# Optimization experiments

Measured on AMD Instinct MI355X. Metric: run time of the kernel, lower is better.

Reference implementation:

```python
import jax, jax.numpy as jnp
import numpy as np

VOCAB = 1_000_000
EMBED_DIM = 128
BATCH = 16_384
NOISE_COUNT = 16


def setup_inputs() -> dict:
    key = jax.random.key(0)
    k1, k2, k3, k4, k5, k6 = jax.random.split(key, 6)
    embed = jax.random.uniform(k1, (EMBED_DIM, VOCAB), jnp.float32, -1.0, 1.0)
    bias = jax.random.uniform(k2, (VOCAB, 1), jnp.float32, -1.0, 1.0)
    u = jax.random.uniform(k3, (VOCAB,), jnp.float32, 1e-3, 1.0)
    freq = u / u.sum()  # normalized unigram^0.75 noise distribution
    targets = jax.random.randint(k4, (BATCH,), 0, VOCAB)
    contexts = jax.random.randint(k5, (BATCH,), 0, VOCAB)
    noises = jax.random.randint(k6, (BATCH * NOISE_COUNT,), 0, VOCAB)
    return {"embed": embed, "bias": bias, "freq": freq,
            "targets": targets, "contexts": contexts, "noises": noises,
            "noise_count": NOISE_COUNT}


def reference(embed, bias, freq, targets, contexts, noises, noise_count):
    # embed: (E, V); bias: (V, 1); freq: (V,)
    E = embed.shape[0]
    B = targets.shape[0]
    re = 10.0
    q = embed[:, targets]                      # (E, B) target embeddings
    r = embed[:, contexts]                     # (E, B) context embeddings
    b = bias[targets, 0][None, :]              # (1, B)
    s = ((r * q).sum(0)[None, :] + b) / E      # (1, B) scaled score
    # positive term: log(sigmoid(s - log(k * p(target))))
    pos = jax.nn.log_sigmoid(s - jnp.log(noise_count * freq[targets]))
    loss = pos.sum()
    # noise term: log(1 - sigmoid(tile(s,k) - log(k * p(noise)))) = log_sigmoid(-x)
    s_tiled = jnp.tile(s, (1, noise_count))    # (1, B*k) == torch.cat((s,)*k, dim=1)
    noise_loss = jax.nn.log_sigmoid(-(s_tiled - jnp.log(noise_count * freq[noises]))).sum()
    total_loss = -(loss + noise_loss) / B
    penalty = re * ((q * q).sum() + (r * r).sum()) / (E * B)
    return total_loss + penalty
```

## Files before the change

### kernel.cpp

```cpp
#include <hip/hip_runtime.h>
#include <hip/hip_bf16.h>
#include <math.h>


#define NB 2048

struct alignas(16) bf16x8 { __hip_bfloat16 h[8]; };

__device__ __forceinline__ float log_sigmoid_f(float x) {
    return fminf(x, 0.0f) - log1pf(expf(-fabsf(x)));
}

__device__ __forceinline__ int task_col(int i, const int* __restrict__ targets,
                                        const int* __restrict__ contexts) {
    const int pair = i >> 1;
    return (i & 1) ? contexts[pair] : targets[pair];
}

__global__ __launch_bounds__(256) void hist_kernel(
    const int* __restrict__ targets, const int* __restrict__ contexts,
    int* __restrict__ counts, int T2, int sh)
{
    const int i = blockIdx.x * 256 + threadIdx.x;
    if (i < T2) atomicAdd(&counts[task_col(i, targets, contexts) >> sh], 1);
}

__global__ __launch_bounds__(256) void scan_kernel(
    const int* __restrict__ counts, int* __restrict__ cursors, int nb)
{
    __shared__ int wv_tot[4];
    const int tid  = threadIdx.x;
    const int lane = tid & 63;
    const int w    = tid >> 6;
    int v[8];
    const int base = tid * 8;
    int local = 0;
    #pragma unroll
    for (int k = 0; k < 8; ++k) {
        const int idx = base + k;
        v[k] = (idx < nb) ? counts[idx] : 0;
        local += v[k];
    }
    int incl = local;
    #pragma unroll
    for (int off = 1; off < 64; off <<= 1) {
        const int n = __shfl_up(incl, off, 64);
        if (lane >= off) incl += n;
    }
    if (lane == 63) wv_tot[w] = incl;
    __syncthreads();
    int wpre = 0;
    for (int i = 0; i < w; ++i) wpre += wv_tot[i];
    int run = wpre + incl - local;
    #pragma unroll
    for (int k = 0; k < 8; ++k) {
        const int idx = base + k;
        if (idx < nb) cursors[idx] = run;
        run += v[k];
    }
}

__global__ __launch_bounds__(256) void scatter_kernel(
    const int* __restrict__ targets, const int* __restrict__ contexts,
    int* __restrict__ cursors, int* __restrict__ sorted,
    int* __restrict__ invperm, int T2, int sh)
{
    const int i = blockIdx.x * 256 + threadIdx.x;
    if (i < T2) {
        const int col = task_col(i, targets, contexts);
        const int pos = atomicAdd(&cursors[col >> sh], 1);
        sorted[pos] = i;
        invperm[i]  = pos;
    }
}

__global__ __launch_bounds__(256) void gather_kernel(
    const float* __restrict__ embed,
    const int* __restrict__ targets, const int* __restrict__ contexts,
    const int* __restrict__ sorted, bf16x8* __restrict__ dense,
    int V, int T2)
{
    const int g = threadIdx.x & 15;
    const int p = threadIdx.x >> 4;
    const int pos = blockIdx.x * 16 + p;
    if (pos >= T2) return;
    const int col = task_col(sorted[pos], targets, contexts);
    const float* src = embed + col + (size_t)(g * 8) * V;
    float v[8];
    #pragma unroll
    for (int k = 0; k < 8; ++k) v[k] = src[(size_t)k * V];
    bf16x8 outv;
    #pragma unroll
    for (int k = 0; k < 8; ++k) outv.h[k] = __float2bfloat16(v[k]);
    dense[(size_t)pos * 16 + g] = outv;
}

__global__ __launch_bounds__(256) void compute_kernel(
    const bf16x8* __restrict__ dense, const int* __restrict__ invperm,
    const float* __restrict__ bias, const float* __restrict__ freq,
    const int* __restrict__ targets, const int* __restrict__ noises,
    float* __restrict__ partials, int B, int NC)
{
    __shared__ float sh_dot[16][17];
    __shared__ float sh_sq [16][17];
    __shared__ float sh_s  [16];
    __shared__ float sh_wred[4];

    const int p = threadIdx.x & 15;
    const int g = threadIdx.x >> 4;
    const int j = blockIdx.x * 16 + p;
    const bool valid = (j < B);

    float contrib = 0.0f;
    float dot = 0.0f, sq = 0.0f;
    float lg0 = 0.0f; bool has0 = false;
    float bval = 0.0f, lgt = 0.0f;

    if (valid) {
        if (g < NC) {
            const int n = noises[j + (size_t)g * B];
            lg0 = logf((float)NC * freq[n]);
            has0 = true;
        }
        if (g == 0) {
            const int t = targets[j];
            bval = bias[t];
            lgt  = logf((float)NC * freq[t]);
        }
        const bf16x8 qv = dense[(size_t)invperm[2 * j]     * 16 + g];
        const bf16x8 rv = dense[(size_t)invperm[2 * j + 1] * 16 + g];
        #pragma unroll
        for (int k = 0; k < 8; ++k) {
            const float qe = __bfloat162float(qv.h[k]);
            const float re = __bfloat162float(rv.h[k]);
            dot = fmaf(qe, re, dot);
            sq  = fmaf(qe, qe, fmaf(re, re, sq));
        }
    }
    sh_dot[p][g] = dot;
    sh_sq [p][g] = sq;
    __syncthreads();

    if (threadIdx.x < 16) {
        float d = 0.0f, s2 = 0.0f;
        #pragma unroll
        for (int gg = 0; gg < 16; ++gg) {
            d  += sh_dot[threadIdx.x][gg];
            s2 += sh_sq [threadIdx.x][gg];
        }
        float sval = 0.0f;
        if (valid) {
            sval = (d + bval) / 128.0f;
            const float pos = log_sigmoid_f(sval - lgt);
            contrib += -pos / (float)B + 10.0f * s2 / (128.0f * (float)B);
        }
        sh_s[threadIdx.x] = sval;
    }
    __syncthreads();

    if (valid) {
        const float sval = sh_s[p];
        float nacc = 0.0f;
        if (has0) nacc = log_sigmoid_f(-(sval - lg0));
        for (int k = g + 16; k < NC; k += 16) {
            const int n = noises[j + (size_t)k * B];
            nacc += log_sigmoid_f(-(sval - logf((float)NC * freq[n])));
        }
        contrib += -nacc / (float)B;
    }

    #pragma unroll
    for (int off = 32; off > 0; off >>= 1)
        contrib += __shfl_xor(contrib, off, 64);
    if ((threadIdx.x & 63) == 0) sh_wred[threadIdx.x >> 6] = contrib;
    __syncthreads();
    if (threadIdx.x == 0)
        partials[blockIdx.x] = sh_wred[0] + sh_wred[1] + sh_wred[2] + sh_wred[3];
}

__global__ __launch_bounds__(256) void reduce_partials_kernel(
    const float* __restrict__ parts, int n, float* __restrict__ out)
{
    __shared__ double sh[256];
    double a = 0.0;
    for (int i = threadIdx.x; i < n; i += 256) a += (double)parts[i];
    sh[threadIdx.x] = a;
    __syncthreads();
    for (int s = 128; s > 0; s >>= 1) {
        if (threadIdx.x < s) sh[threadIdx.x] += sh[threadIdx.x + s];
        __syncthreads();
    }
    if (threadIdx.x == 0) out[0] = (float)sh[0];
}

__global__ __launch_bounds__(256) void nce_fallback(
    const float* __restrict__ embed, const float* __restrict__ bias,
    const float* __restrict__ freq, const int* __restrict__ targets,
    const int* __restrict__ contexts, const int* __restrict__ noises,
    float* __restrict__ block_partials, int V, int E, int B, int NC)
{
    __shared__ float sh_dot[16][17];
    __shared__ float sh_sq [16][17];
    __shared__ float sh_s  [16];
    __shared__ float sh_wred[4];
    const int p = threadIdx.x & 15;
    const int g = threadIdx.x >> 4;
    const int j = blockIdx.x * 16 + p;
    const bool valid = (j < B);
    float contrib = 0.0f, dot = 0.0f, sq = 0.0f;
    float lg0 = 0.0f; bool has0 = false; float bval = 0.0f, lgt = 0.0f;
    if (valid) {
        const int t = targets[j], c = contexts[j];
        if (g < NC) { const int n = noises[j + (size_t)g * B];
                      lg0 = logf((float)NC * freq[n]); has0 = true; }
        if (g == 0) { bval = bias[t]; lgt = logf((float)NC * freq[t]); }
        const int epc = E / 16, e0 = g * epc;
        const float* ct = embed + t; const float* cc = embed + c;
        #pragma unroll 8
        for (int e = e0; e < e0 + epc; ++e) {
            float qe = ct[(size_t)e * V], re = cc[(size_t)e * V];
            dot = fmaf(qe, re, dot);
            sq  = fmaf(qe, qe, fmaf(re, re, sq));
        }
    }
    sh_dot[p][g] = dot; sh_sq[p][g] = sq;
    __syncthreads();
    if (threadIdx.x < 16) {
        float d = 0.0f, s2 = 0.0f;
        #pragma unroll
        for (int gg = 0; gg < 16; ++gg) { d += sh_dot[threadIdx.x][gg]; s2 += sh_sq[threadIdx.x][gg]; }
        float sval = 0.0f;
        if (valid) {
            sval = (d + bval) / (float)E;
            contrib += -log_sigmoid_f(sval - lgt) / (float)B + 10.0f * s2 / ((float)E * (float)B);
        }
        sh_s[threadIdx.x] = sval;
    }
    __syncthreads();
    if (valid) {
        const float sval = sh_s[p];
        float nacc = 0.0f;
        if (has0) nacc = log_sigmoid_f(-(sval - lg0));
        for (int k = g + 16; k < NC; k += 16) {
            const int n = noises[j + (size_t)k * B];
            nacc += log_sigmoid_f(-(sval - logf((float)NC * freq[n])));
        }
        contrib += -nacc / (float)B;
    }
    #pragma unroll
    for (int off = 32; off > 0; off >>= 1) contrib += __shfl_xor(contrib, off, 64);
    if ((threadIdx.x & 63) == 0) sh_wred[threadIdx.x >> 6] = contrib;
    __syncthreads();
    if (threadIdx.x == 0)
        block_partials[blockIdx.x] = sh_wred[0] + sh_wred[1] + sh_wred[2] + sh_wred[3];
}

extern "C" void kernel_launch(void* const* d_in, const int* in_sizes, int n_in,
                              void* d_out, int out_size, void* d_ws, size_t ws_size,
                              hipStream_t stream) {
    const float* embed    = (const float*)d_in[0];
    const float* bias     = (const float*)d_in[1];
    const float* freq     = (const float*)d_in[2];
    const int*   targets  = (const int*)d_in[3];
    const int*   contexts = (const int*)d_in[4];
    const int*   noises   = (const int*)d_in[5];

    const int V  = in_sizes[2];
    const int E  = in_sizes[0] / V;
    const int B  = in_sizes[3];
    const int NC = in_sizes[5] / B;
    const int T2 = 2 * B;

    char* ws = (char*)d_ws;
    float* partials = (float*)ws;
    int*   counts   = (int*)(ws + 16384);
    int*   cursors  = counts + NB;
    int*   sorted   = cursors + NB;
    int*   invperm  = sorted + T2;
    size_t dense_off = 16384 + 2 * (size_t)NB * 4 + 2 * (size_t)T2 * 4;
    dense_off = (dense_off + 255) & ~(size_t)255;
    bf16x8* dense = (bf16x8*)(ws + dense_off);
    const size_t needed = dense_off + (size_t)T2 * 128 * 2;

    const int nblocks = (B + 15) / 16;

    if (E == 128 && (B & 15) == 0 && ws_size >= needed) {
        int sh = 0;
        while ((((V - 1) >> sh) + 1) > NB) ++sh;
        const int nb = ((V - 1) >> sh) + 1;

        hipMemsetAsync(counts, 0, (size_t)NB * 4, stream);
        hist_kernel<<<(T2 + 255) / 256, 256, 0, stream>>>(targets, contexts, counts, T2, sh);
        scan_kernel<<<1, 256, 0, stream>>>(counts, cursors, nb);
        scatter_kernel<<<(T2 + 255) / 256, 256, 0, stream>>>(targets, contexts, cursors,
                                                             sorted, invperm, T2, sh);
        gather_kernel<<<(T2 + 15) / 16, 256, 0, stream>>>(embed, targets, contexts,
                                                          sorted, dense, V, T2);
        compute_kernel<<<nblocks, 256, 0, stream>>>(dense, invperm, bias, freq,
                                                    targets, noises, partials, B, NC);
    } else {
        nce_fallback<<<nblocks, 256, 0, stream>>>(embed, bias, freq, targets, contexts,
                                                  noises, partials, V, E, B, NC);
    }
    reduce_partials_kernel<<<1, 256, 0, stream>>>(partials, nblocks, (float*)d_out);
}
```

Measured before the change: 102.2 us.

## Gather embedding rows into transposed bf16 buffer with row-parallel grid

The gather stage now gives each thread one sorted column. The grid is split across embedding-dimension slices, and each slice writes its values into a transposed (E, T2) bf16 buffer, so reads of a given embedding row across consecutive sorted columns fall near each other. The scatter stage now stores the column index itself rather than the task index, which drops one indirection in the gather. The compute kernel reads the transposed buffer with strided scalar bf16 loads instead of 16-byte vector loads, so the compute side gets less coalescing in exchange for better gather locality.

```diff
diff --git a/kernel.cpp b/kernel.cpp
--- a/kernel.cpp
+++ b/kernel.cpp
@@ -4,8 +4,7 @@
 
 
 #define NB 2048
-
-struct alignas(16) bf16x8 { __hip_bfloat16 h[8]; };
+#define ELOOP 8
 
 __device__ __forceinline__ float log_sigmoid_f(float x) {
     return fminf(x, 0.0f) - log1pf(expf(-fabsf(x)));
@@ -62,44 +61,40 @@
 
 __global__ __launch_bounds__(256) void scatter_kernel(
     const int* __restrict__ targets, const int* __restrict__ contexts,
-    int* __restrict__ cursors, int* __restrict__ sorted,
+    int* __restrict__ cursors, int* __restrict__ sorted_cols,
     int* __restrict__ invperm, int T2, int sh)
 {
     const int i = blockIdx.x * 256 + threadIdx.x;
     if (i < T2) {
         const int col = task_col(i, targets, contexts);
         const int pos = atomicAdd(&cursors[col >> sh], 1);
-        sorted[pos] = i;
+        sorted_cols[pos] = col;
         invperm[i]  = pos;
     }
 }
 
-__global__ __launch_bounds__(256) void gather_kernel(
-    const float* __restrict__ embed,
-    const int* __restrict__ targets, const int* __restrict__ contexts,
-    const int* __restrict__ sorted, bf16x8* __restrict__ dense,
-    int V, int T2)
-{
-    const int g = threadIdx.x & 15;
-    const int p = threadIdx.x >> 4;
-    const int pos = blockIdx.x * 16 + p;
+__global__ __launch_bounds__(256) void gather_rows_kernel(
+    const float* __restrict__ embed, const int* __restrict__ sorted_cols,
+    __hip_bfloat16* __restrict__ denseT, int V, int T2)
+{
+    const int pos = blockIdx.x * 256 + threadIdx.x;
     if (pos >= T2) return;
-    const int col = task_col(sorted[pos], targets, contexts);
-    const float* src = embed + col + (size_t)(g * 8) * V;
-    float v[8];
-    #pragma unroll
-    for (int k = 0; k < 8; ++k) v[k] = src[(size_t)k * V];
-    bf16x8 outv;
-    #pragma unroll
-    for (int k = 0; k < 8; ++k) outv.h[k] = __float2bfloat16(v[k]);
-    dense[(size_t)pos * 16 + g] = outv;
+    const int col = sorted_cols[pos];
+    const int e0  = blockIdx.y * ELOOP;
+    const float* src = embed + (size_t)e0 * V + col;
+    float v[ELOOP];
+    #pragma unroll
+    for (int k = 0; k < ELOOP; ++k) v[k] = src[(size_t)k * V];
+    __hip_bfloat16* dst = denseT + (size_t)e0 * T2 + pos;
+    #pragma unroll
+    for (int k = 0; k < ELOOP; ++k) dst[(size_t)k * T2] = __float2bfloat16(v[k]);
 }
 
 __global__ __launch_bounds__(256) void compute_kernel(
-    const bf16x8* __restrict__ dense, const int* __restrict__ invperm,
+    const __hip_bfloat16* __restrict__ denseT, const int* __restrict__ invperm,
     const float* __restrict__ bias, const float* __restrict__ freq,
     const int* __restrict__ targets, const int* __restrict__ noises,
-    float* __restrict__ partials, int B, int NC)
+    float* __restrict__ partials, int B, int NC, int T2)
 {
     __shared__ float sh_dot[16][17];
     __shared__ float sh_sq [16][17];
@@ -127,12 +122,14 @@
             bval = bias[t];
             lgt  = logf((float)NC * freq[t]);
         }
-        const bf16x8 qv = dense[(size_t)invperm[2 * j]     * 16 + g];
-        const bf16x8 rv = dense[(size_t)invperm[2 * j + 1] * 16 + g];
+        const int pq = invperm[2 * j];
+        const int pr = invperm[2 * j + 1];
+        const __hip_bfloat16* bq = denseT + (size_t)(g * 8) * T2 + pq;
+        const __hip_bfloat16* br = denseT + (size_t)(g * 8) * T2 + pr;
         #pragma unroll
         for (int k = 0; k < 8; ++k) {
-            const float qe = __bfloat162float(qv.h[k]);
-            const float re = __bfloat162float(rv.h[k]);
+            const float qe = __bfloat162float(bq[(size_t)k * T2]);
+            const float re = __bfloat162float(br[(size_t)k * T2]);
             dot = fmaf(qe, re, dot);
             sq  = fmaf(qe, qe, fmaf(re, re, sq));
         }
@@ -275,16 +272,16 @@
     float* partials = (float*)ws;
     int*   counts   = (int*)(ws + 16384);
     int*   cursors  = counts + NB;
-    int*   sorted   = cursors + NB;
-    int*   invperm  = sorted + T2;
+    int*   sorted_cols = cursors + NB;
+    int*   invperm  = sorted_cols + T2;
     size_t dense_off = 16384 + 2 * (size_t)NB * 4 + 2 * (size_t)T2 * 4;
     dense_off = (dense_off + 255) & ~(size_t)255;
-    bf16x8* dense = (bf16x8*)(ws + dense_off);
-    const size_t needed = dense_off + (size_t)T2 * 128 * 2;
+    __hip_bfloat16* denseT = (__hip_bfloat16*)(ws + dense_off);
+    const size_t needed = dense_off + (size_t)E * T2 * 2;
 
     const int nblocks = (B + 15) / 16;
 
-    if (E == 128 && (B & 15) == 0 && ws_size >= needed) {
+    if (E == 128 && (T2 & 255) == 0 && ws_size >= needed) {
         int sh = 0;
         while ((((V - 1) >> sh) + 1) > NB) ++sh;
         const int nb = ((V - 1) >> sh) + 1;
@@ -293,11 +290,11 @@
         hist_kernel<<<(T2 + 255) / 256, 256, 0, stream>>>(targets, contexts, counts, T2, sh);
         scan_kernel<<<1, 256, 0, stream>>>(counts, cursors, nb);
         scatter_kernel<<<(T2 + 255) / 256, 256, 0, stream>>>(targets, contexts, cursors,
-                                                             sorted, invperm, T2, sh);
-        gather_kernel<<<(T2 + 15) / 16, 256, 0, stream>>>(embed, targets, contexts,
-                                                          sorted, dense, V, T2);
-        compute_kernel<<<nblocks, 256, 0, stream>>>(dense, invperm, bias, freq,
-                                                    targets, noises, partials, B, NC);
+                                                             sorted_cols, invperm, T2, sh);
+        dim3 ggrid(T2 / 256, E / ELOOP);
+        gather_rows_kernel<<<ggrid, 256, 0, stream>>>(embed, sorted_cols, denseT, V, T2);
+        compute_kernel<<<nblocks, 256, 0, stream>>>(denseT, invperm, bias, freq,
+                                                    targets, noises, partials, B, NC, T2);
     } else {
         nce_fallback<<<nblocks, 256, 0, stream>>>(embed, bias, freq, targets, contexts,
                                                   noises, partials, V, E, B, NC);
```

New measurement: 119.3 us. 16.8% more time.

## Gather embeddings with 64 adjacent sorted columns per wave and LDS transpose

Applied to the files above, without the earlier changes.

The scatter now stores the column index directly, which removes the indirect targets/contexts lookup in the gather. The gather is restructured so that each wavefront's 64 lanes read 64 consecutive sorted columns for the same embedding row, giving nearby addresses per load instead of 16 scattered columns. Results go through a shared-memory tile and are written out as 16-byte row chunks in the existing dense layout. This adds a block barrier and an LDS round trip, and the 2D grid reloads sorted_cols once per embedding slice.

```diff
diff --git a/kernel.cpp b/kernel.cpp
--- a/kernel.cpp
+++ b/kernel.cpp
@@ -4,6 +4,8 @@
 
 
 #define NB 2048
+#define GP 64
+#define GE 32
 
 struct alignas(16) bf16x8 { __hip_bfloat16 h[8]; };
 
@@ -62,37 +64,54 @@
 
 __global__ __launch_bounds__(256) void scatter_kernel(
     const int* __restrict__ targets, const int* __restrict__ contexts,
-    int* __restrict__ cursors, int* __restrict__ sorted,
+    int* __restrict__ cursors, int* __restrict__ sorted_cols,
     int* __restrict__ invperm, int T2, int sh)
 {
     const int i = blockIdx.x * 256 + threadIdx.x;
     if (i < T2) {
         const int col = task_col(i, targets, contexts);
         const int pos = atomicAdd(&cursors[col >> sh], 1);
-        sorted[pos] = i;
+        sorted_cols[pos] = col;
         invperm[i]  = pos;
     }
 }
 
-__global__ __launch_bounds__(256) void gather_kernel(
-    const float* __restrict__ embed,
-    const int* __restrict__ targets, const int* __restrict__ contexts,
-    const int* __restrict__ sorted, bf16x8* __restrict__ dense,
-    int V, int T2)
-{
-    const int g = threadIdx.x & 15;
-    const int p = threadIdx.x >> 4;
-    const int pos = blockIdx.x * 16 + p;
-    if (pos >= T2) return;
-    const int col = task_col(sorted[pos], targets, contexts);
-    const float* src = embed + col + (size_t)(g * 8) * V;
+__global__ __launch_bounds__(256) void gather_t_kernel(
+    const float* __restrict__ embed, const int* __restrict__ sorted_cols,
+    __hip_bfloat16* __restrict__ dense, int V, int E)
+{
+    __shared__ unsigned int tile[GP][17];
+
+    const int pos_l = threadIdx.x & 63;
+    const int eg    = threadIdx.x >> 6;
+    const int pos   = blockIdx.x * GP + pos_l;
+    const int e0    = blockIdx.y * GE;
+    const int col   = sorted_cols[pos];
+
+    const float* src = embed + (size_t)(e0 + eg * 8) * V + col;
     float v[8];
     #pragma unroll
     for (int k = 0; k < 8; ++k) v[k] = src[(size_t)k * V];
-    bf16x8 outv;
-    #pragma unroll
-    for (int k = 0; k < 8; ++k) outv.h[k] = __float2bfloat16(v[k]);
-    dense[(size_t)pos * 16 + g] = outv;
+
+    #pragma unroll
+    for (int kk = 0; kk < 4; ++kk) {
+        union { __hip_bfloat16 h[2]; unsigned int u; } cvt;
+        cvt.h[0] = __float2bfloat16(v[2 * kk]);
+        cvt.h[1] = __float2bfloat16(v[2 * kk + 1]);
+        tile[pos_l][eg * 4 + kk] = cvt.u;
+    }
+    __syncthreads();
+
+    const int pos_w = threadIdx.x >> 2;
+    const int c4    = threadIdx.x & 3;
+    uint4 w;
+    w.x = tile[pos_w][c4 * 4 + 0];
+    w.y = tile[pos_w][c4 * 4 + 1];
+    w.z = tile[pos_w][c4 * 4 + 2];
+    w.w = tile[pos_w][c4 * 4 + 3];
+    unsigned int* drow = (unsigned int*)dense
+        + (size_t)(blockIdx.x * GP + pos_w) * (E / 2) + (e0 / 2) + c4 * 4;
+    *(uint4*)drow = w;
 }
 
 __global__ __launch_bounds__(256) void compute_kernel(
@@ -275,16 +294,16 @@
     float* partials = (float*)ws;
     int*   counts   = (int*)(ws + 16384);
     int*   cursors  = counts + NB;
-    int*   sorted   = cursors + NB;
-    int*   invperm  = sorted + T2;
+    int*   sorted_cols = cursors + NB;
+    int*   invperm  = sorted_cols + T2;
     size_t dense_off = 16384 + 2 * (size_t)NB * 4 + 2 * (size_t)T2 * 4;
     dense_off = (dense_off + 255) & ~(size_t)255;
-    bf16x8* dense = (bf16x8*)(ws + dense_off);
-    const size_t needed = dense_off + (size_t)T2 * 128 * 2;
+    __hip_bfloat16* dense = (__hip_bfloat16*)(ws + dense_off);
+    const size_t needed = dense_off + (size_t)T2 * E * 2;
 
     const int nblocks = (B + 15) / 16;
 
-    if (E == 128 && (B & 15) == 0 && ws_size >= needed) {
+    if (E == 128 && (T2 % GP) == 0 && ws_size >= needed) {
         int sh = 0;
         while ((((V - 1) >> sh) + 1) > NB) ++sh;
         const int nb = ((V - 1) >> sh) + 1;
@@ -293,11 +312,13 @@
         hist_kernel<<<(T2 + 255) / 256, 256, 0, stream>>>(targets, contexts, counts, T2, sh);
         scan_kernel<<<1, 256, 0, stream>>>(counts, cursors, nb);
         scatter_kernel<<<(T2 + 255) / 256, 256, 0, stream>>>(targets, contexts, cursors,
-                                                             sorted, invperm, T2, sh);
-        gather_kernel<<<(T2 + 15) / 16, 256, 0, stream>>>(embed, targets, contexts,
-                                                          sorted, dense, V, T2);
-        compute_kernel<<<nblocks, 256, 0, stream>>>(dense, invperm, bias, freq,
-                                                    targets, noises, partials, B, NC);
+                                                             sorted_cols, invperm, T2, sh);
+        dim3 ggrid(T2 / GP, E / GE);
+        gather_t_kernel<<<ggrid, 256, 0, stream>>>(embed, sorted_cols,
+                                                   dense, V, E);
+        compute_kernel<<<nblocks, 256, 0, stream>>>((const bf16x8*)dense, invperm,
+                                                    bias, freq, targets, noises,
+                                                    partials, B, NC);
     } else {
         nce_fallback<<<nblocks, 256, 0, stream>>>(embed, bias, freq, targets, contexts,
                                                   noises, partials, V, E, B, NC);
```

After: 94.36 us. 1.08x faster.
